# Kernel optimization log

Measured on AMD Instinct MI355X. Metric: run time of the kernel, lower is better.

The kernel has to match this reference:

```python
import jax, jax.numpy as jnp
import numpy as np

S, H, I, E, K = 16384, 1024, 512, 64, 2
CAP = 640  # capacity per expert: ceil(S*K/E * 1.25)


def setup_inputs() -> dict:
    key = jax.random.key(0)
    k0, k1, k2, k3, k4 = jax.random.split(key, 5)
    x = jax.random.normal(k0, (S, H), jnp.float32)
    w_gate = jax.random.normal(k1, (H, E), jnp.float32) * 0.02
    wg = jax.random.normal(k2, (E, H, I), jnp.float32) * 0.02
    wu = jax.random.normal(k3, (E, H, I), jnp.float32) * 0.02
    wd = jax.random.normal(k4, (E, I, H), jnp.float32) * 0.02
    return {"x": x, "w_gate": w_gate, "wg": wg, "wu": wu, "wd": wd}


def reference(x, w_gate, wg, wu, wd):
    # --- gate (fp32) + softmax ---
    logits = x.astype(jnp.float32) @ w_gate                      # [S,E]
    prob = jax.nn.softmax(logits, axis=-1)
    topk_p, topk_e = jax.lax.top_k(prob, K)                      # [S,K]

    # --- capacity-based dispatch (token-major, route-minor order, as in torch loop) ---
    flat_e = topk_e.reshape(-1)                                  # [S*K]
    onehot = jax.nn.one_hot(flat_e, E, dtype=jnp.int32)          # [S*K,E]
    pos = jnp.cumsum(onehot, axis=0)[jnp.arange(S * K), flat_e] - 1  # slot within expert
    valid = pos < CAP                                            # [S*K]

    combine_w = jnp.where(valid.reshape(S, K), topk_p, 0.0)      # dropped -> 0 weight
    slot_idx = jnp.where(valid, flat_e * CAP + pos, E * CAP)     # dummy row for drops
    x_rep = jnp.repeat(x, K, axis=0)                             # [S*K,H], row i = x[i//K]
    y = jnp.zeros((E * CAP + 1, H), x.dtype).at[slot_idx].set(x_rep)[: E * CAP]
    dispatched = y.reshape(E, CAP, H)

    # --- per-expert SwiGLU MLP (grouped GEMMs) ---
    g = jnp.einsum("ech,ehi->eci", dispatched, wg)
    u = jnp.einsum("ech,ehi->eci", dispatched, wu)
    expert_out = jnp.einsum("eci,eih->ech", jax.nn.silu(g) * u, wd)  # [E,CAP,H]

    # --- normalize weights and combine (gather + weighted sum) ---
    cw = combine_w / jnp.clip(combine_w.sum(-1, keepdims=True), 1e-12, None)
    scatter_index = jnp.where(valid, flat_e * CAP + pos, -1).reshape(S, K)
    gathered = expert_out.reshape(E * CAP, H)[scatter_index]     # [S,K,H]; -1 wraps, weight=0
    out = jnp.einsum("sk,skh->sh", cw, gathered)                 # [S,H]

    router_loss = jnp.zeros((1,), jnp.float32)
    return out, cw, router_loss, logits
```

## Files before the change

### kernel.cpp

```cpp
#include <hip/hip_runtime.h>
#include <hip/hip_bf16.h>

constexpr int S_TOK = 16384;
constexpr int HDIM  = 1024;
constexpr int IDIM  = 512;
constexpr int NEXP  = 64;
constexpr int CAPC  = 640;
constexpr int NCHUNK = 128;

typedef __attribute__((ext_vector_type(8))) short bf16x8;
typedef __attribute__((ext_vector_type(4))) short short4v;
typedef __attribute__((ext_vector_type(16))) float f32x16;

__device__ __forceinline__ float bf2f(unsigned short u){
  return __uint_as_float(((unsigned)u) << 16);
}
__device__ __forceinline__ unsigned short f2bf(float f){
  unsigned u = __float_as_uint(f);
  return (unsigned short)((u + 0x7fffu + ((u >> 16) & 1u)) >> 16);
}
__device__ __forceinline__ unsigned pk2cvt(float a, float b){
  unsigned r;
  asm volatile("v_cvt_pk_bf16_f32 %0, %1, %2" : "=v"(r) : "v"(a), "v"(b));
  return r;
}
__device__ __forceinline__ void gload_lds16(const void* g, void* l){
  __builtin_amdgcn_global_load_lds((const __attribute__((address_space(1))) unsigned*)g,
                                   (__attribute__((address_space(3))) unsigned*)l, 16, 0, 0);
}
__device__ __forceinline__ unsigned ldsoff(const void* p){ return (unsigned)(size_t)p; }
__device__ __forceinline__ void trread2(unsigned addr, short4v& lo, short4v& hi){
  asm volatile("ds_read_b64_tr_b16 %0, %2\n\t"
               "ds_read_b64_tr_b16 %1, %2 offset:128"
               : "=&v"(lo), "=&v"(hi) : "v"(addr));
}

__global__ __launch_bounds__(256) void gate_kernel(
    const float* __restrict__ x, const float* __restrict__ wgate,
    float* __restrict__ logits_out, float* __restrict__ topk_p,
    int* __restrict__ flat_e, float* __restrict__ rl_out)
{
  __shared__ float xs[4][HDIM];
  const int w = threadIdx.x >> 6, lane = threadIdx.x & 63;
  const int tok = blockIdx.x * 4 + w;
  const float4* xr = (const float4*)(x + (size_t)tok * HDIM);
  float4* xd = (float4*)(&xs[w][0]);
#pragma unroll
  for (int j = 0; j < 4; ++j) xd[j * 64 + lane] = xr[j * 64 + lane];
  __syncthreads();
  float a0 = 0.f, a1 = 0.f, a2 = 0.f, a3 = 0.f;
#pragma unroll 4
  for (int h = 0; h < HDIM; h += 4){
    a0 = fmaf(xs[w][h],     wgate[(h)     * NEXP + lane], a0);
    a1 = fmaf(xs[w][h + 1], wgate[(h + 1) * NEXP + lane], a1);
    a2 = fmaf(xs[w][h + 2], wgate[(h + 2) * NEXP + lane], a2);
    a3 = fmaf(xs[w][h + 3], wgate[(h + 3) * NEXP + lane], a3);
  }
  float acc = (a0 + a1) + (a2 + a3);
  logits_out[(size_t)tok * NEXP + lane] = acc;
  float m = acc;
#pragma unroll
  for (int d = 1; d < 64; d <<= 1) m = fmaxf(m, __shfl_xor(m, d));
  float p = expf(acc - m);
  float sum = p;
#pragma unroll
  for (int d = 1; d < 64; d <<= 1) sum += __shfl_xor(sum, d);
  float prob = p / sum;
  float v = prob; int idx = lane;
#pragma unroll
  for (int d = 1; d < 64; d <<= 1){
    float ov = __shfl_xor(v, d); int oi = __shfl_xor(idx, d);
    if (ov > v || (ov == v && oi < idx)){ v = ov; idx = oi; }
  }
  const int e1 = idx; const float p1 = v;
  v = (lane == e1) ? -1.f : prob; idx = lane;
#pragma unroll
  for (int d = 1; d < 64; d <<= 1){
    float ov = __shfl_xor(v, d); int oi = __shfl_xor(idx, d);
    if (ov > v || (ov == v && oi < idx)){ v = ov; idx = oi; }
  }
  if (lane == 0){
    flat_e[tok * 2]     = e1;  flat_e[tok * 2 + 1] = idx;
    topk_p[tok * 2]     = p1;  topk_p[tok * 2 + 1] = v;
  }
  if (tok == 0 && lane == 0) rl_out[0] = 0.f;
}

__global__ __launch_bounds__(256) void hist_kernel(const int* __restrict__ flat_e,
                                                   int* __restrict__ counts)
{
  __shared__ int hh[NEXP];
  const int t = threadIdx.x;
  if (t < NEXP) hh[t] = 0;
  __syncthreads();
  const int e = flat_e[blockIdx.x * 256 + t];
  atomicAdd(&hh[e], 1);
  __syncthreads();
  if (t < NEXP) counts[blockIdx.x * NEXP + t] = hh[t];
}

__global__ __launch_bounds__(256) void offsets_kernel(const int* __restrict__ counts,
                                                      int* __restrict__ offs,
                                                      int* __restrict__ etot)
{
  const int w = threadIdx.x >> 6, lane = threadIdx.x & 63;
  const int e = blockIdx.x * 4 + w;
  int v0 = counts[lane * NEXP + e];
  int v1 = counts[(64 + lane) * NEXP + e];
  int s0 = v0, s1 = v1;
#pragma unroll
  for (int d = 1; d < 64; d <<= 1){
    int n0 = __shfl_up(s0, d); if (lane >= d) s0 += n0;
    int n1 = __shfl_up(s1, d); if (lane >= d) s1 += n1;
  }
  const int tot0 = __shfl(s0, 63);
  offs[lane * NEXP + e]        = s0 - v0;
  offs[(64 + lane) * NEXP + e] = tot0 + s1 - v1;
  if (lane == 63) etot[e] = tot0 + s1;
}

__global__ __launch_bounds__(256) void place_kernel(
    const int* __restrict__ flat_e, const float* __restrict__ topk_p,
    const int* __restrict__ offs, int* __restrict__ entry_slot,
    int* __restrict__ token_of_slot, float* __restrict__ cw_out)
{
  __shared__ int es[256];
  __shared__ float wsh[256];
  const int t = threadIdx.x;
  const int i = blockIdx.x * 256 + t;
  const int e = flat_e[i];
  es[t] = e;
  __syncthreads();
  int local = 0;
  for (int j = 0; j < t; ++j) local += (es[j] == e);
  const int pos = offs[blockIdx.x * NEXP + e] + local;
  const bool valid = pos < CAPC;
  const int slot = e * CAPC + pos;
  entry_slot[i] = valid ? slot : -1;
  if (valid) token_of_slot[slot] = i >> 1;
  const float p = topk_p[i];
  wsh[t] = valid ? p : 0.f;
  __syncthreads();
  const float wme = wsh[t], wo = wsh[t ^ 1];
  cw_out[i] = wme / fmaxf(wme + wo, 1e-12f);
}

__global__ __launch_bounds__(256) void adisp_kernel(
    const float* __restrict__ x, const int* __restrict__ token_of_slot,
    const int* __restrict__ etot, unsigned short* __restrict__ adisp)
{
  const int slot = blockIdx.x;
  const int e = slot / CAPC, c = slot - e * CAPC;
  int cnt = etot[e]; if (cnt > CAPC) cnt = CAPC;
  if (c >= cnt) return;
  const int tok = token_of_slot[slot];
  const int t = threadIdx.x;
  float4 v = ((const float4*)(x + (size_t)tok * HDIM))[t];
  ushort4 o; o.x = f2bf(v.x); o.y = f2bf(v.y); o.z = f2bf(v.z); o.w = f2bf(v.w);
  ((ushort4*)(adisp + (size_t)slot * HDIM))[t] = o;
}


__global__ __launch_bounds__(512) void gemm1_kernel(
    const unsigned short* __restrict__ adisp,
    const float* __restrict__ wg, const float* __restrict__ wu,
    const int* __restrict__ etot,
    unsigned short* __restrict__ hbuf)
{
  constexpr int NK1 = HDIM / 32;
  __shared__ unsigned short As[2][256 * 32];
  __shared__ unsigned short Bs[2][2 * 128 * 32];
  const int bb = blockIdx.x;
  const int lb = (bb & 7) * 96 + (bb >> 3);
  const int e = lb / 12; const int r2 = lb - e * 12;
  const int nt = r2 / 3, mt = r2 - nt * 3;
  { int cnt = etot[e]; if (cnt > CAPC) cnt = CAPC;
    if (mt * 256 >= cnt) return; }
  const int t = threadIdx.x, w = t >> 6, lane = t & 63;
  const int wr = w >> 2, wc = w & 3;
  const size_t arow0 = (size_t)e * CAPC + (size_t)mt * 256;
  const unsigned short* abase = adisp + arow0 * HDIM;
  const float* gsrc = wg + (size_t)e * HDIM * IDIM + nt * 128;
  const float* usrc = wu + (size_t)e * HDIM * IDIM + nt * 128;

  int aoff[2];
#pragma unroll
  for (int rr = 0; rr < 2; ++rr){
    int c = rr * 512 + t;
    int row = c >> 2;
    if (mt * 256 + row >= CAPC) row = 0;
    int jsrc = (c & 3) ^ ((row >> 1) & 3);
    aoff[rr] = row * HDIM + jsrc * 8;
  }
  const int ks_ = w >> 2, khalf = (w >> 1) & 1, par = w & 1;
  const int dk = (lane >> 1) & 3, h8 = lane & 1;
  const int n16 = (lane >> 3) & 1, n32 = lane >> 4;
  const int bk = 16 * ks_ + 8 * khalf + 4 * par + dk;
  const int bn0 = n32 * 32 + n16 * 16 + h8 * 8;
  const int bgo = bk * IDIM + bn0;
  const unsigned bwo = (unsigned)(n32 * 1024 + ks_ * 512 + (khalf * 2 + n16) * 128
                                  + par * 64 + dk * 16 + h8 * 8);

  f32x16 ag[4], au[4];
#pragma unroll
  for (int i = 0; i < 4; ++i)
#pragma unroll
    for (int q = 0; q < 16; ++q){ ag[i][q] = 0.f; au[i][q] = 0.f; }

  float4 g0a, g0b, u0a, u0b, g1a, g1b, u1a, u1b;

#define G1_LOAD(KB, RA, RB, RC, RD) {                                          \
    const float* gp_ = gsrc + (size_t)(KB) * IDIM + bgo;                       \
    const float* up_ = usrc + (size_t)(KB) * IDIM + bgo;                       \
    RA = *(const float4*)gp_;       RB = *(const float4*)(gp_ + 4);            \
    RC = *(const float4*)up_;       RD = *(const float4*)(up_ + 4); }

#define G1_STORE(NB, WA, WB, WC, WD) {                                         \
    *(uint4*)&Bs[NB][bwo] = make_uint4(pk2cvt(WA.x,WA.y), pk2cvt(WA.z,WA.w),   \
                                       pk2cvt(WB.x,WB.y), pk2cvt(WB.z,WB.w));  \
    *(uint4*)&Bs[NB][4096 + bwo] = make_uint4(pk2cvt(WC.x,WC.y), pk2cvt(WC.z,WC.w), \
                                       pk2cvt(WD.x,WD.y), pk2cvt(WD.z,WD.w)); }

#define G1_STEP(TI, LA, LB, LC, LD, WA, WB, WC, WD) {                          \
    const int cur_ = (TI) & 1;                                                 \
    const bool pfA_ = (TI) + 1 < NK1;                                          \
    const bool pfB_ = (TI) + 2 < NK1;                                          \
    if (pfA_){                                                                 \
      const int kb1_ = ((TI) + 1) * 32;                                        \
      gload_lds16(abase + aoff[0] + kb1_, &As[((TI) + 1) & 1][(w * 64) * 8]);  \
      gload_lds16(abase + aoff[1] + kb1_, &As[((TI) + 1) & 1][(512 + w * 64) * 8]); \
    }                                                                          \
    if (pfB_){ G1_LOAD(((TI) + 2) * 32, LA, LB, LC, LD); }                     \
    const unsigned b0_ = ldsoff(&Bs[cur_][0]) + (unsigned)wc * 2048            \
                         + (unsigned)(lane >> 4) * 256 + (unsigned)(lane & 15) * 8; \
    _Pragma("unroll")                                                          \
    for (int ksi = 0; ksi < 2; ++ksi){                                         \
      bf16x8 af_[4], bg_, bu_;                                                 \
      { int koct_ = ksi * 2 + (lane >> 5);                                     \
        _Pragma("unroll")                                                      \
        for (int mp = 0; mp < 4; ++mp){                                        \
          int row_ = wr * 128 + mp * 32 + (lane & 31);                         \
          af_[mp] = *(const bf16x8*)&As[cur_][row_ * 32 + ((koct_ ^ ((row_ >> 1) & 3)) * 8)]; \
        } }                                                                    \
      { short4v l0_, l1_, m0_, m1_;                                            \
        trread2(b0_ + (unsigned)ksi * 1024, l0_, l1_);                         \
        bg_ = __builtin_shufflevector(l0_, l1_, 0,1,2,3,4,5,6,7);              \
        trread2(b0_ + 8192 + (unsigned)ksi * 1024, m0_, m1_);                  \
        bu_ = __builtin_shufflevector(m0_, m1_, 0,1,2,3,4,5,6,7); }            \
      asm volatile("s_waitcnt lgkmcnt(0)" ::: "memory");                       \
      __builtin_amdgcn_sched_barrier(0);                                       \
      __builtin_amdgcn_s_setprio(1);                                           \
      _Pragma("unroll")                                                        \
      for (int mp = 0; mp < 4; ++mp){                                          \
        ag[mp] = __builtin_amdgcn_mfma_f32_32x32x16_bf16(af_[mp], bg_, ag[mp], 0, 0, 0); \
        au[mp] = __builtin_amdgcn_mfma_f32_32x32x16_bf16(af_[mp], bu_, au[mp], 0, 0, 0); \
      }                                                                        \
      __builtin_amdgcn_s_setprio(0);                                           \
    }                                                                          \
    if (pfA_){                                                                 \
      if (pfB_) asm volatile("s_waitcnt vmcnt(4)" ::: "memory");               \
      else      asm volatile("s_waitcnt vmcnt(0)" ::: "memory");               \
      G1_STORE(((TI) + 1) & 1, WA, WB, WC, WD);                                \
    }                                                                          \
    asm volatile("s_waitcnt lgkmcnt(0)" ::: "memory");                         \
    __builtin_amdgcn_s_barrier();                                              \
    __builtin_amdgcn_sched_barrier(0);                                         \
  }

  gload_lds16(abase + aoff[0] + 0,  &As[0][(w * 64) * 8]);
  gload_lds16(abase + aoff[1] + 0,  &As[0][(512 + w * 64) * 8]);
  G1_LOAD(0,  g0a, g0b, u0a, u0b);
  G1_LOAD(32, g1a, g1b, u1a, u1b);
  asm volatile("s_waitcnt vmcnt(4)" ::: "memory");
  G1_STORE(0, g0a, g0b, u0a, u0b);
  asm volatile("s_waitcnt lgkmcnt(0)" ::: "memory");
  __builtin_amdgcn_s_barrier();

  for (int tb = 0; tb < NK1; tb += 2){
    G1_STEP(tb,     g0a, g0b, u0a, u0b,  g1a, g1b, u1a, u1b);
    G1_STEP(tb + 1, g1a, g1b, u1a, u1b,  g0a, g0b, u0a, u0b);
  }
#undef G1_STEP
#undef G1_STORE
#undef G1_LOAD

#pragma unroll
  for (int mp = 0; mp < 4; ++mp)
#pragma unroll
    for (int r = 0; r < 16; ++r){
      int row = wr * 128 + mp * 32 + (r & 3) + 8 * (r >> 2) + 4 * (lane >> 5);
      if (mt * 256 + row >= CAPC) continue;
      int col = nt * 128 + wc * 32 + (lane & 31);
      float gv = ag[mp][r], uv = au[mp][r];
      float hv = gv / (1.f + expf(-gv)) * uv;
      hbuf[(arow0 + row) * IDIM + col] = f2bf(hv);
    }
}

__global__ __launch_bounds__(512) void gemm2_kernel(
    const unsigned short* __restrict__ hbuf,
    const float* __restrict__ wd,
    const int* __restrict__ etot,
    unsigned short* __restrict__ eo)
{
  constexpr int NK2 = IDIM / 32;
  __shared__ unsigned short As[2][256 * 32];
  __shared__ unsigned short Bs[2][2 * 128 * 32];
  const int bb = blockIdx.x;
  const int lb = (bb & 7) * 96 + (bb >> 3);
  const int e = lb / 12; const int r2 = lb - e * 12;
  const int nt = r2 / 3, mt = r2 - nt * 3;
  { int cnt = etot[e]; if (cnt > CAPC) cnt = CAPC;
    if (mt * 256 >= cnt) return; }
  const int t = threadIdx.x, w = t >> 6, lane = t & 63;
  const int wr = w >> 2, wc = w & 3;
  const size_t arow0 = (size_t)e * CAPC + (size_t)mt * 256;
  const unsigned short* abase = hbuf + arow0 * IDIM;
  const float* dsrc = wd + (size_t)e * IDIM * HDIM + nt * 256;

  int aoff[2];
#pragma unroll
  for (int rr = 0; rr < 2; ++rr){
    int c = rr * 512 + t;
    int row = c >> 2;
    if (mt * 256 + row >= CAPC) row = 0;
    int jsrc = (c & 3) ^ ((row >> 1) & 3);
    aoff[rr] = row * IDIM + jsrc * 8;
  }
  const int ks_ = w >> 2, khalf = (w >> 1) & 1, par = w & 1;
  const int dk = (lane >> 1) & 3, h8 = lane & 1;
  const int n16 = (lane >> 3) & 1, n32 = lane >> 4;
  const int bk = 16 * ks_ + 8 * khalf + 4 * par + dk;
  const int bn0 = n32 * 32 + n16 * 16 + h8 * 8;
  const int bgo = bk * HDIM + bn0;
  const unsigned bwo = (unsigned)(n32 * 1024 + ks_ * 512 + (khalf * 2 + n16) * 128
                                  + par * 64 + dk * 16 + h8 * 8);

  f32x16 ac[4][2];
#pragma unroll
  for (int i = 0; i < 4; ++i)
#pragma unroll
    for (int j = 0; j < 2; ++j)
#pragma unroll
      for (int q = 0; q < 16; ++q) ac[i][j][q] = 0.f;

  float4 p0a, p0b, p1a, p1b, q0a, q0b, q1a, q1b;

#define G2_LOAD(KB, RA, RB, RC, RD) {                                          \
    const float* gp_ = dsrc + (size_t)(KB) * HDIM + bgo;                       \
    RA = *(const float4*)gp_;         RB = *(const float4*)(gp_ + 4);          \
    RC = *(const float4*)(gp_ + 128); RD = *(const float4*)(gp_ + 132); }

#define G2_STORE(NB, WA, WB, WC, WD) {                                         \
    *(uint4*)&Bs[NB][bwo] = make_uint4(pk2cvt(WA.x,WA.y), pk2cvt(WA.z,WA.w),   \
                                       pk2cvt(WB.x,WB.y), pk2cvt(WB.z,WB.w));  \
    *(uint4*)&Bs[NB][4096 + bwo] = make_uint4(pk2cvt(WC.x,WC.y), pk2cvt(WC.z,WC.w), \
                                       pk2cvt(WD.x,WD.y), pk2cvt(WD.z,WD.w)); }

#define G2_STEP(TI, LA, LB, LC, LD, WA, WB, WC, WD) {                          \
    const int cur_ = (TI) & 1;                                                 \
    const bool pfA_ = (TI) + 1 < NK2;                                          \
    const bool pfB_ = (TI) + 2 < NK2;                                          \
    if (pfA_){                                                                 \
      const int kb1_ = ((TI) + 1) * 32;                                        \
      gload_lds16(abase + aoff[0] + kb1_, &As[((TI) + 1) & 1][(w * 64) * 8]);  \
      gload_lds16(abase + aoff[1] + kb1_, &As[((TI) + 1) & 1][(512 + w * 64) * 8]); \
    }                                                                          \
    if (pfB_){ G2_LOAD(((TI) + 2) * 32, LA, LB, LC, LD); }                     \
    const unsigned b0_ = ldsoff(&Bs[cur_][0]) + (unsigned)wc * 4096            \
                         + (unsigned)(lane >> 4) * 256 + (unsigned)(lane & 15) * 8; \
    _Pragma("unroll")                                                          \
    for (int ksi = 0; ksi < 2; ++ksi){                                         \
      bf16x8 af_[4], b0f_, b1f_;                                               \
      { int koct_ = ksi * 2 + (lane >> 5);                                     \
        _Pragma("unroll")                                                      \
        for (int mp = 0; mp < 4; ++mp){                                        \
          int row_ = wr * 128 + mp * 32 + (lane & 31);                         \
          af_[mp] = *(const bf16x8*)&As[cur_][row_ * 32 + ((koct_ ^ ((row_ >> 1) & 3)) * 8)]; \
        } }                                                                    \
      { short4v l0_, l1_, m0_, m1_;                                            \
        trread2(b0_ + (unsigned)ksi * 1024, l0_, l1_);                         \
        b0f_ = __builtin_shufflevector(l0_, l1_, 0,1,2,3,4,5,6,7);             \
        trread2(b0_ + 2048 + (unsigned)ksi * 1024, m0_, m1_);                  \
        b1f_ = __builtin_shufflevector(m0_, m1_, 0,1,2,3,4,5,6,7); }           \
      asm volatile("s_waitcnt lgkmcnt(0)" ::: "memory");                       \
      __builtin_amdgcn_sched_barrier(0);                                       \
      __builtin_amdgcn_s_setprio(1);                                           \
      _Pragma("unroll")                                                        \
      for (int mp = 0; mp < 4; ++mp){                                          \
        ac[mp][0] = __builtin_amdgcn_mfma_f32_32x32x16_bf16(af_[mp], b0f_, ac[mp][0], 0, 0, 0); \
        ac[mp][1] = __builtin_amdgcn_mfma_f32_32x32x16_bf16(af_[mp], b1f_, ac[mp][1], 0, 0, 0); \
      }                                                                        \
      __builtin_amdgcn_s_setprio(0);                                           \
    }                                                                          \
    if (pfA_){                                                                 \
      if (pfB_) asm volatile("s_waitcnt vmcnt(4)" ::: "memory");               \
      else      asm volatile("s_waitcnt vmcnt(0)" ::: "memory");               \
      G2_STORE(((TI) + 1) & 1, WA, WB, WC, WD);                                \
    }                                                                          \
    asm volatile("s_waitcnt lgkmcnt(0)" ::: "memory");                         \
    __builtin_amdgcn_s_barrier();                                              \
    __builtin_amdgcn_sched_barrier(0);                                         \
  }

  gload_lds16(abase + aoff[0] + 0,  &As[0][(w * 64) * 8]);
  gload_lds16(abase + aoff[1] + 0,  &As[0][(512 + w * 64) * 8]);
  G2_LOAD(0,  p0a, p0b, q0a, q0b);
  G2_LOAD(32, p1a, p1b, q1a, q1b);
  asm volatile("s_waitcnt vmcnt(4)" ::: "memory");
  G2_STORE(0, p0a, p0b, q0a, q0b);
  asm volatile("s_waitcnt lgkmcnt(0)" ::: "memory");
  __builtin_amdgcn_s_barrier();

  for (int tb = 0; tb < NK2; tb += 2){
    G2_STEP(tb,     p0a, p0b, q0a, q0b,  p1a, p1b, q1a, q1b);
    G2_STEP(tb + 1, p1a, p1b, q1a, q1b,  p0a, p0b, q0a, q0b);
  }
#undef G2_STEP
#undef G2_STORE
#undef G2_LOAD

#pragma unroll
  for (int mp = 0; mp < 4; ++mp)
#pragma unroll
    for (int np = 0; np < 2; ++np)
#pragma unroll
      for (int r = 0; r < 16; ++r){
        int row = wr * 128 + mp * 32 + (r & 3) + 8 * (r >> 2) + 4 * (lane >> 5);
        if (mt * 256 + row >= CAPC) continue;
        int col = nt * 256 + wc * 64 + np * 32 + (lane & 31);
        eo[(arow0 + row) * HDIM + col] = f2bf(ac[mp][np][r]);
      }
}

__global__ __launch_bounds__(256) void combine_kernel(
    const unsigned short* __restrict__ eo, const int* __restrict__ entry_slot,
    const float* __restrict__ cw, float* __restrict__ out)
{
  const int s = blockIdx.x, t = threadIdx.x;
  const int s0 = entry_slot[2 * s], s1 = entry_slot[2 * s + 1];
  const float w0 = cw[2 * s], w1 = cw[2 * s + 1];
  const int c = t * 4;
  float r0 = 0.f, r1 = 0.f, r2 = 0.f, r3 = 0.f;
  if (s0 >= 0){
    ushort4 vq = *(const ushort4*)&eo[(size_t)s0 * HDIM + c];
    r0 += w0 * bf2f(vq.x); r1 += w0 * bf2f(vq.y); r2 += w0 * bf2f(vq.z); r3 += w0 * bf2f(vq.w);
  }
  if (s1 >= 0){
    ushort4 vq = *(const ushort4*)&eo[(size_t)s1 * HDIM + c];
    r0 += w1 * bf2f(vq.x); r1 += w1 * bf2f(vq.y); r2 += w1 * bf2f(vq.z); r3 += w1 * bf2f(vq.w);
  }
  ((float4*)(out + (size_t)s * HDIM))[t] = make_float4(r0, r1, r2, r3);
}

extern "C" void kernel_launch(void* const* d_in, const int* in_sizes, int n_in,
                              void* d_out, int out_size, void* d_ws, size_t ws_size,
                              hipStream_t stream) {
  (void)in_sizes; (void)n_in; (void)out_size; (void)ws_size;
  const float* x     = (const float*)d_in[0];
  const float* wgate = (const float*)d_in[1];
  const float* wg    = (const float*)d_in[2];
  const float* wu    = (const float*)d_in[3];
  const float* wd    = (const float*)d_in[4];

  float* out        = (float*)d_out;
  float* cw_out     = out + (size_t)S_TOK * HDIM;
  float* rl_out     = cw_out + (size_t)S_TOK * 2;
  float* logits_out = rl_out + 1;

  char* w8 = (char*)d_ws;
  size_t off = 0;
  auto alloc = [&](size_t bytes){ size_t r = off; off += (bytes + 255) & ~(size_t)255; return r; };
  int*   flat_e_ws        = (int*)  (w8 + alloc((size_t)32768 * 4));
  float* topk_p_ws        = (float*)(w8 + alloc((size_t)32768 * 4));
  int*   counts_ws        = (int*)  (w8 + alloc((size_t)NCHUNK * NEXP * 4));
  int*   offs_ws          = (int*)  (w8 + alloc((size_t)NCHUNK * NEXP * 4));
  int*   etot_ws          = (int*)  (w8 + alloc((size_t)NEXP * 4));
  int*   entry_slot_ws    = (int*)  (w8 + alloc((size_t)32768 * 4));
  int*   token_of_slot_ws = (int*)  (w8 + alloc((size_t)NEXP * CAPC * 4));
  unsigned short* hbuf_ws = (unsigned short*)(w8 + alloc((size_t)NEXP * CAPC * IDIM * 2));
  unsigned short* adisp_ws= (unsigned short*)(w8 + alloc((size_t)NEXP * CAPC * HDIM * 2));
  unsigned short* eo_ws   = adisp_ws;

  gate_kernel   <<<S_TOK / 4, 256, 0, stream>>>(x, wgate, logits_out, topk_p_ws, flat_e_ws, rl_out);
  hist_kernel   <<<NCHUNK,    256, 0, stream>>>(flat_e_ws, counts_ws);
  offsets_kernel<<<16,        256, 0, stream>>>(counts_ws, offs_ws, etot_ws);
  place_kernel  <<<NCHUNK,    256, 0, stream>>>(flat_e_ws, topk_p_ws, offs_ws,
                                                entry_slot_ws, token_of_slot_ws, cw_out);
  adisp_kernel  <<<NEXP * CAPC, 256, 0, stream>>>(x, token_of_slot_ws, etot_ws, adisp_ws);
  gemm1_kernel  <<<NEXP * 12, 512, 0, stream>>>(adisp_ws, wg, wu, etot_ws, hbuf_ws);
  gemm2_kernel  <<<NEXP * 12, 512, 0, stream>>>(hbuf_ws, wd, etot_ws, eo_ws);
  combine_kernel<<<S_TOK,     256, 0, stream>>>(eo_ws, entry_slot_ws, cw_out, out);
}
```

Before: 475.5 us.

## Fuse combine into down-projection GEMM epilogue via weighted atomic scatter-add

The separate combine kernel and the bf16 expert-output buffer are removed. The gemm2 epilogue now scales each output row by its per-slot combine weight and atomically adds it into the fp32 output row of the owning token, which is zeroed up front with a memset. This drops one full write and read of the expert-output tensor and one kernel launch. In exchange it adds a full memset of the output plus float atomics with scattered, row-granular access, and summation order is no longer deterministic.

```diff
diff --git a/kernel.cpp b/kernel.cpp
--- a/kernel.cpp
+++ b/kernel.cpp
@@ -121,8 +121,8 @@
 
 __global__ __launch_bounds__(256) void place_kernel(
     const int* __restrict__ flat_e, const float* __restrict__ topk_p,
-    const int* __restrict__ offs, int* __restrict__ entry_slot,
-    int* __restrict__ token_of_slot, float* __restrict__ cw_out)
+    const int* __restrict__ offs, int* __restrict__ token_of_slot,
+    float* __restrict__ slot_w, float* __restrict__ cw_out)
 {
   __shared__ int es[256];
   __shared__ float wsh[256];
@@ -136,13 +136,14 @@
   const int pos = offs[blockIdx.x * NEXP + e] + local;
   const bool valid = pos < CAPC;
   const int slot = e * CAPC + pos;
-  entry_slot[i] = valid ? slot : -1;
   if (valid) token_of_slot[slot] = i >> 1;
   const float p = topk_p[i];
   wsh[t] = valid ? p : 0.f;
   __syncthreads();
   const float wme = wsh[t], wo = wsh[t ^ 1];
-  cw_out[i] = wme / fmaxf(wme + wo, 1e-12f);
+  const float cw = wme / fmaxf(wme + wo, 1e-12f);
+  cw_out[i] = cw;
+  if (valid) slot_w[slot] = cw;
 }
 
 __global__ __launch_bounds__(256) void adisp_kernel(
@@ -301,7 +302,9 @@
     const unsigned short* __restrict__ hbuf,
     const float* __restrict__ wd,
     const int* __restrict__ etot,
-    unsigned short* __restrict__ eo)
+    const int* __restrict__ token_of_slot,
+    const float* __restrict__ slot_w,
+    float* __restrict__ out)
 {
   constexpr int NK2 = IDIM / 32;
   __shared__ unsigned short As[2][256 * 32];
@@ -310,8 +313,9 @@
   const int lb = (bb & 7) * 96 + (bb >> 3);
   const int e = lb / 12; const int r2 = lb - e * 12;
   const int nt = r2 / 3, mt = r2 - nt * 3;
+  int cnt_;
   { int cnt = etot[e]; if (cnt > CAPC) cnt = CAPC;
-    if (mt * 256 >= cnt) return; }
+    if (mt * 256 >= cnt) return; cnt_ = cnt; }
   const int t = threadIdx.x, w = t >> 6, lane = t & 63;
   const int wr = w >> 2, wc = w & 3;
   const size_t arow0 = (size_t)e * CAPC + (size_t)mt * 256;
@@ -423,34 +427,19 @@
 #pragma unroll
   for (int mp = 0; mp < 4; ++mp)
 #pragma unroll
-    for (int np = 0; np < 2; ++np)
-#pragma unroll
-      for (int r = 0; r < 16; ++r){
-        int row = wr * 128 + mp * 32 + (r & 3) + 8 * (r >> 2) + 4 * (lane >> 5);
-        if (mt * 256 + row >= CAPC) continue;
+    for (int r = 0; r < 16; ++r){
+      int row = wr * 128 + mp * 32 + (r & 3) + 8 * (r >> 2) + 4 * (lane >> 5);
+      if (mt * 256 + row >= cnt_) continue;
+      const int slotg = (int)(arow0 + row) ;
+      const int tok = token_of_slot[slotg];
+      const float wgt = slot_w[slotg];
+      float* orow = out + (size_t)tok * HDIM;
+#pragma unroll
+      for (int np = 0; np < 2; ++np){
         int col = nt * 256 + wc * 64 + np * 32 + (lane & 31);
-        eo[(arow0 + row) * HDIM + col] = f2bf(ac[mp][np][r]);
+        atomicAdd(&orow[col], wgt * ac[mp][np][r]);
       }
-}
-
-__global__ __launch_bounds__(256) void combine_kernel(
-    const unsigned short* __restrict__ eo, const int* __restrict__ entry_slot,
-    const float* __restrict__ cw, float* __restrict__ out)
-{
-  const int s = blockIdx.x, t = threadIdx.x;
-  const int s0 = entry_slot[2 * s], s1 = entry_slot[2 * s + 1];
-  const float w0 = cw[2 * s], w1 = cw[2 * s + 1];
-  const int c = t * 4;
-  float r0 = 0.f, r1 = 0.f, r2 = 0.f, r3 = 0.f;
-  if (s0 >= 0){
-    ushort4 vq = *(const ushort4*)&eo[(size_t)s0 * HDIM + c];
-    r0 += w0 * bf2f(vq.x); r1 += w0 * bf2f(vq.y); r2 += w0 * bf2f(vq.z); r3 += w0 * bf2f(vq.w);
-  }
-  if (s1 >= 0){
-    ushort4 vq = *(const ushort4*)&eo[(size_t)s1 * HDIM + c];
-    r0 += w1 * bf2f(vq.x); r1 += w1 * bf2f(vq.y); r2 += w1 * bf2f(vq.z); r3 += w1 * bf2f(vq.w);
-  }
-  ((float4*)(out + (size_t)s * HDIM))[t] = make_float4(r0, r1, r2, r3);
+    }
 }
 
 extern "C" void kernel_launch(void* const* d_in, const int* in_sizes, int n_in,
@@ -476,19 +465,20 @@
   int*   counts_ws        = (int*)  (w8 + alloc((size_t)NCHUNK * NEXP * 4));
   int*   offs_ws          = (int*)  (w8 + alloc((size_t)NCHUNK * NEXP * 4));
   int*   etot_ws          = (int*)  (w8 + alloc((size_t)NEXP * 4));
-  int*   entry_slot_ws    = (int*)  (w8 + alloc((size_t)32768 * 4));
   int*   token_of_slot_ws = (int*)  (w8 + alloc((size_t)NEXP * CAPC * 4));
+  float* slot_w_ws        = (float*)(w8 + alloc((size_t)NEXP * CAPC * 4));
   unsigned short* hbuf_ws = (unsigned short*)(w8 + alloc((size_t)NEXP * CAPC * IDIM * 2));
   unsigned short* adisp_ws= (unsigned short*)(w8 + alloc((size_t)NEXP * CAPC * HDIM * 2));
-  unsigned short* eo_ws   = adisp_ws;
+
+  hipMemsetAsync(out, 0, (size_t)S_TOK * HDIM * sizeof(float), stream);
 
   gate_kernel   <<<S_TOK / 4, 256, 0, stream>>>(x, wgate, logits_out, topk_p_ws, flat_e_ws, rl_out);
   hist_kernel   <<<NCHUNK,    256, 0, stream>>>(flat_e_ws, counts_ws);
   offsets_kernel<<<16,        256, 0, stream>>>(counts_ws, offs_ws, etot_ws);
   place_kernel  <<<NCHUNK,    256, 0, stream>>>(flat_e_ws, topk_p_ws, offs_ws,
-                                                entry_slot_ws, token_of_slot_ws, cw_out);
+                                                token_of_slot_ws, slot_w_ws, cw_out);
   adisp_kernel  <<<NEXP * CAPC, 256, 0, stream>>>(x, token_of_slot_ws, etot_ws, adisp_ws);
   gemm1_kernel  <<<NEXP * 12, 512, 0, stream>>>(adisp_ws, wg, wu, etot_ws, hbuf_ws);
-  gemm2_kernel  <<<NEXP * 12, 512, 0, stream>>>(hbuf_ws, wd, etot_ws, eo_ws);
-  combine_kernel<<<S_TOK,     256, 0, stream>>>(eo_ws, entry_slot_ws, cw_out, out);
-}
+  gemm2_kernel  <<<NEXP * 12, 512, 0, stream>>>(hbuf_ws, wd, etot_ws,
+                                                token_of_slot_ws, slot_w_ws, out);
+}
```

Measured after the change: 566.0 us. 19.0% more time.

## Fuse token gather and bf16 conversion into gemm1 A-operand loads

Applied to the files above, without the earlier changes.

Removes the separate adisp kernel that gathered dispatched tokens into a bf16 staging buffer. gemm1 now looks up token_of_slot itself, loads fp32 rows of x straight through registers, converts them to bf16 and writes them to swizzled LDS, double-buffered alongside the weight loads. This drops one launch and a write-then-read of the bf16 staging buffer. In exchange each gemm1 block re-reads fp32 x (twice the bytes of bf16), the same rows are read again by every N-tile block, and register pressure rises because the direct LDS loads are replaced by register staging.

```diff
diff --git a/kernel.cpp b/kernel.cpp
--- a/kernel.cpp
+++ b/kernel.cpp
@@ -145,24 +145,9 @@
   cw_out[i] = wme / fmaxf(wme + wo, 1e-12f);
 }
 
-__global__ __launch_bounds__(256) void adisp_kernel(
+
+__global__ __launch_bounds__(512) void gemm1_kernel(
     const float* __restrict__ x, const int* __restrict__ token_of_slot,
-    const int* __restrict__ etot, unsigned short* __restrict__ adisp)
-{
-  const int slot = blockIdx.x;
-  const int e = slot / CAPC, c = slot - e * CAPC;
-  int cnt = etot[e]; if (cnt > CAPC) cnt = CAPC;
-  if (c >= cnt) return;
-  const int tok = token_of_slot[slot];
-  const int t = threadIdx.x;
-  float4 v = ((const float4*)(x + (size_t)tok * HDIM))[t];
-  ushort4 o; o.x = f2bf(v.x); o.y = f2bf(v.y); o.z = f2bf(v.z); o.w = f2bf(v.w);
-  ((ushort4*)(adisp + (size_t)slot * HDIM))[t] = o;
-}
-
-
-__global__ __launch_bounds__(512) void gemm1_kernel(
-    const unsigned short* __restrict__ adisp,
     const float* __restrict__ wg, const float* __restrict__ wu,
     const int* __restrict__ etot,
     unsigned short* __restrict__ hbuf)
@@ -174,23 +159,26 @@
   const int lb = (bb & 7) * 96 + (bb >> 3);
   const int e = lb / 12; const int r2 = lb - e * 12;
   const int nt = r2 / 3, mt = r2 - nt * 3;
+  int cnt_;
   { int cnt = etot[e]; if (cnt > CAPC) cnt = CAPC;
-    if (mt * 256 >= cnt) return; }
+    if (mt * 256 >= cnt) return; cnt_ = cnt; }
   const int t = threadIdx.x, w = t >> 6, lane = t & 63;
   const int wr = w >> 2, wc = w & 3;
   const size_t arow0 = (size_t)e * CAPC + (size_t)mt * 256;
-  const unsigned short* abase = adisp + arow0 * HDIM;
   const float* gsrc = wg + (size_t)e * HDIM * IDIM + nt * 128;
   const float* usrc = wu + (size_t)e * HDIM * IDIM + nt * 128;
 
-  int aoff[2];
-#pragma unroll
-  for (int rr = 0; rr < 2; ++rr){
-    int c = rr * 512 + t;
-    int row = c >> 2;
-    if (mt * 256 + row >= CAPC) row = 0;
-    int jsrc = (c & 3) ^ ((row >> 1) & 3);
-    aoff[rr] = row * HDIM + jsrc * 8;
+  const float* asrc0; const float* asrc1;
+  unsigned awr0, awr1;
+  {
+    int c = t, row = c >> 2;
+    int tok = (mt * 256 + row < cnt_) ? token_of_slot[arow0 + row] : 0;
+    asrc0 = x + (size_t)tok * HDIM + (c & 3) * 8;
+    awr0 = (unsigned)(row * 32 + (((c & 3) ^ ((row >> 1) & 3)) * 8));
+    c = 512 + t; row = c >> 2;
+    tok = (mt * 256 + row < cnt_) ? token_of_slot[arow0 + row] : 0;
+    asrc1 = x + (size_t)tok * HDIM + (c & 3) * 8;
+    awr1 = (unsigned)(row * 32 + (((c & 3) ^ ((row >> 1) & 3)) * 8));
   }
   const int ks_ = w >> 2, khalf = (w >> 1) & 1, par = w & 1;
   const int dk = (lane >> 1) & 3, h8 = lane & 1;
@@ -207,7 +195,18 @@
 #pragma unroll
     for (int q = 0; q < 16; ++q){ ag[i][q] = 0.f; au[i][q] = 0.f; }
 
+  float4 xA0, xA1, xA2, xA3, yA0, yA1, yA2, yA3;
   float4 g0a, g0b, u0a, u0b, g1a, g1b, u1a, u1b;
+
+#define A_LOAD(KB, R0, R1, R2, R3) {                                           \
+    R0 = *(const float4*)(asrc0 + (KB));  R1 = *(const float4*)(asrc0 + (KB) + 4); \
+    R2 = *(const float4*)(asrc1 + (KB));  R3 = *(const float4*)(asrc1 + (KB) + 4); }
+
+#define A_STORE(NB, R0, R1, R2, R3) {                                          \
+    *(uint4*)&As[NB][awr0] = make_uint4(pk2cvt(R0.x,R0.y), pk2cvt(R0.z,R0.w),  \
+                                        pk2cvt(R1.x,R1.y), pk2cvt(R1.z,R1.w)); \
+    *(uint4*)&As[NB][awr1] = make_uint4(pk2cvt(R2.x,R2.y), pk2cvt(R2.z,R2.w),  \
+                                        pk2cvt(R3.x,R3.y), pk2cvt(R3.z,R3.w)); }
 
 #define G1_LOAD(KB, RA, RB, RC, RD) {                                          \
     const float* gp_ = gsrc + (size_t)(KB) * IDIM + bgo;                       \
@@ -221,16 +220,13 @@
     *(uint4*)&Bs[NB][4096 + bwo] = make_uint4(pk2cvt(WC.x,WC.y), pk2cvt(WC.z,WC.w), \
                                        pk2cvt(WD.x,WD.y), pk2cvt(WD.z,WD.w)); }
 
-#define G1_STEP(TI, LA, LB, LC, LD, WA, WB, WC, WD) {                          \
+#define G1_STEP(TI, LX0,LX1,LX2,LX3, LA,LB,LC,LD, SX0,SX1,SX2,SX3, WA,WB,WC,WD) { \
     const int cur_ = (TI) & 1;                                                 \
-    const bool pfA_ = (TI) + 1 < NK1;                                          \
-    const bool pfB_ = (TI) + 2 < NK1;                                          \
-    if (pfA_){                                                                 \
-      const int kb1_ = ((TI) + 1) * 32;                                        \
-      gload_lds16(abase + aoff[0] + kb1_, &As[((TI) + 1) & 1][(w * 64) * 8]);  \
-      gload_lds16(abase + aoff[1] + kb1_, &As[((TI) + 1) & 1][(512 + w * 64) * 8]); \
-    }                                                                          \
-    if (pfB_){ G1_LOAD(((TI) + 2) * 32, LA, LB, LC, LD); }                     \
+    const bool pf_ = (TI) + 2 < NK1;                                           \
+    if (pf_){                                                                  \
+      A_LOAD(((TI) + 2) * 32, LX0, LX1, LX2, LX3);                             \
+      G1_LOAD(((TI) + 2) * 32, LA, LB, LC, LD);                                \
+    }                                                                          \
     const unsigned b0_ = ldsoff(&Bs[cur_][0]) + (unsigned)wc * 2048            \
                          + (unsigned)(lane >> 4) * 256 + (unsigned)(lane & 15) * 8; \
     _Pragma("unroll")                                                          \
@@ -257,9 +253,10 @@
       }                                                                        \
       __builtin_amdgcn_s_setprio(0);                                           \
     }                                                                          \
-    if (pfA_){                                                                 \
-      if (pfB_) asm volatile("s_waitcnt vmcnt(4)" ::: "memory");               \
-      else      asm volatile("s_waitcnt vmcnt(0)" ::: "memory");               \
+    if ((TI) + 1 < NK1){                                                       \
+      if (pf_) asm volatile("s_waitcnt vmcnt(8)" ::: "memory");                \
+      else     asm volatile("s_waitcnt vmcnt(0)" ::: "memory");                \
+      A_STORE(((TI) + 1) & 1, SX0, SX1, SX2, SX3);                             \
       G1_STORE(((TI) + 1) & 1, WA, WB, WC, WD);                                \
     }                                                                          \
     asm volatile("s_waitcnt lgkmcnt(0)" ::: "memory");                         \
@@ -267,22 +264,27 @@
     __builtin_amdgcn_sched_barrier(0);                                         \
   }
 
-  gload_lds16(abase + aoff[0] + 0,  &As[0][(w * 64) * 8]);
-  gload_lds16(abase + aoff[1] + 0,  &As[0][(512 + w * 64) * 8]);
+  A_LOAD(0,  xA0, xA1, xA2, xA3);
   G1_LOAD(0,  g0a, g0b, u0a, u0b);
+  A_LOAD(32, yA0, yA1, yA2, yA3);
   G1_LOAD(32, g1a, g1b, u1a, u1b);
-  asm volatile("s_waitcnt vmcnt(4)" ::: "memory");
+  asm volatile("s_waitcnt vmcnt(8)" ::: "memory");
+  A_STORE(0, xA0, xA1, xA2, xA3);
   G1_STORE(0, g0a, g0b, u0a, u0b);
   asm volatile("s_waitcnt lgkmcnt(0)" ::: "memory");
   __builtin_amdgcn_s_barrier();
 
   for (int tb = 0; tb < NK1; tb += 2){
-    G1_STEP(tb,     g0a, g0b, u0a, u0b,  g1a, g1b, u1a, u1b);
-    G1_STEP(tb + 1, g1a, g1b, u1a, u1b,  g0a, g0b, u0a, u0b);
+    G1_STEP(tb,     xA0, xA1, xA2, xA3,  g0a, g0b, u0a, u0b,
+                    yA0, yA1, yA2, yA3,  g1a, g1b, u1a, u1b);
+    G1_STEP(tb + 1, yA0, yA1, yA2, yA3,  g1a, g1b, u1a, u1b,
+                    xA0, xA1, xA2, xA3,  g0a, g0b, u0a, u0b);
   }
 #undef G1_STEP
 #undef G1_STORE
 #undef G1_LOAD
+#undef A_STORE
+#undef A_LOAD
 
 #pragma unroll
   for (int mp = 0; mp < 4; ++mp)
@@ -479,16 +481,14 @@
   int*   entry_slot_ws    = (int*)  (w8 + alloc((size_t)32768 * 4));
   int*   token_of_slot_ws = (int*)  (w8 + alloc((size_t)NEXP * CAPC * 4));
   unsigned short* hbuf_ws = (unsigned short*)(w8 + alloc((size_t)NEXP * CAPC * IDIM * 2));
-  unsigned short* adisp_ws= (unsigned short*)(w8 + alloc((size_t)NEXP * CAPC * HDIM * 2));
-  unsigned short* eo_ws   = adisp_ws;
+  unsigned short* eo_ws   = (unsigned short*)(w8 + alloc((size_t)NEXP * CAPC * HDIM * 2));
 
   gate_kernel   <<<S_TOK / 4, 256, 0, stream>>>(x, wgate, logits_out, topk_p_ws, flat_e_ws, rl_out);
   hist_kernel   <<<NCHUNK,    256, 0, stream>>>(flat_e_ws, counts_ws);
   offsets_kernel<<<16,        256, 0, stream>>>(counts_ws, offs_ws, etot_ws);
   place_kernel  <<<NCHUNK,    256, 0, stream>>>(flat_e_ws, topk_p_ws, offs_ws,
                                                 entry_slot_ws, token_of_slot_ws, cw_out);
-  adisp_kernel  <<<NEXP * CAPC, 256, 0, stream>>>(x, token_of_slot_ws, etot_ws, adisp_ws);
-  gemm1_kernel  <<<NEXP * 12, 512, 0, stream>>>(adisp_ws, wg, wu, etot_ws, hbuf_ws);
+  gemm1_kernel  <<<NEXP * 12, 512, 0, stream>>>(x, token_of_slot_ws, wg, wu, etot_ws, hbuf_ws);
   gemm2_kernel  <<<NEXP * 12, 512, 0, stream>>>(hbuf_ws, wd, etot_ws, eo_ws);
   combine_kernel<<<S_TOK,     256, 0, stream>>>(eo_ws, entry_slot_ws, cw_out, out);
 }
```

Measured after the change: 441.6 us, median of 2. 1.08x faster.
